# Optimization experiments

Hardware: AMD Instinct MI355X
Metric: run time of the kernel (lower is better)

The kernel has to match this reference:

```python
import jax, jax.numpy as jnp
import numpy as np

# FTDEA(e_hidden=300, r_hidden=100, t_hidden=100)
N_NODES = 50000
N_EDGES = 250000
N_EDGES_ALL = 500000
N_REL = 300
EH, RH, TH = 300, 100, 100


def _seg_softmax(logits, seg, num):
    # torch_geometric.utils.softmax: segment-wise stable softmax
    m = jax.ops.segment_max(logits, seg, num_segments=num)
    e = jnp.exp(logits - m[seg])
    s = jax.ops.segment_sum(e, seg, num_segments=num)
    return e / s[seg]


def _gcn(x, j, i, n):
    deg = jax.ops.segment_sum(jnp.ones(i.shape[0], x.dtype), i, num_segments=n)
    dinv = jnp.where(deg > 0, 1.0 / jnp.sqrt(jnp.maximum(deg, 1.0)), 0.0)
    norm = dinv[j] * dinv[i]
    return jax.nn.relu(jax.ops.segment_sum(norm[:, None] * x[j], i, num_segments=n))


def setup_inputs():
    key = jax.random.key(0)
    ks = jax.random.split(key, 32)
    f32 = jnp.float32

    def w(k, shape):
        return jax.random.normal(k, shape, f32) / np.float32(np.sqrt(shape[0]))

    inp = {
        "x": jax.random.normal(ks[0], (N_NODES, EH), f32),
        "edge_index": jax.random.randint(ks[1], (2, N_EDGES), 0, N_NODES),
        "rel": jax.random.randint(ks[2], (N_EDGES,), 0, N_REL),
        "edge_index_all": jax.random.randint(ks[3], (2, N_EDGES_ALL), 0, N_NODES),
        "rel_size": jnp.arange(N_EDGES),
        "hw1_w": w(ks[4], (EH, EH)), "hw1_b": jnp.zeros((EH,), f32),
        "hw2_w": w(ks[5], (EH, EH)), "hw2_b": jnp.zeros((EH,), f32),
        "tc1_w": w(ks[6], (EH, TH)), "tc1_b": jnp.zeros((TH,), f32),
        "sr1_w": w(ks[7], (2 * TH, RH)), "sr1_b": jnp.zeros((RH,), f32),
        "a1_w": w(ks[8], (RH,)), "a5_w": w(ks[9], (RH,)),
        "wr_w": w(ks[10], (RH + 2 * TH, EH)), "wr_b": jnp.zeros((EH,), f32),
        "wr1_w": w(ks[11], (RH + 2 * TH, EH)), "wr1_b": jnp.zeros((EH,), f32),
        "wr2_w": w(ks[12], (RH + 2 * TH, EH)), "wr2_b": jnp.zeros((EH,), f32),
        "ah_w": w(ks[13], (EH,)), "ah1_w": w(ks[14], (EH,)), "at_w": w(ks[15], (EH,)),
        "ar1_w": w(ks[16], (EH,)), "ar2_w": w(ks[17], (EH,)), "ar3_w": w(ks[18], (EH,)),
        "ai_w": w(ks[19], (EH,)), "aj_w": w(ks[20], (EH,)),
        "fc_w": w(ks[21], (2 * EH,)), "fc_b": jnp.zeros((1,), f32),
    }
    return inp


def _forward(x, hw1_w, hw1_b, hw2_w, hw2_b, tc1_w, tc1_b, sr1_w, sr1_b, a1_w, a5_w,
             wr_w, wr_b, wr1_w, wr1_b, wr2_w, wr2_b, ah_w, ah1_w, at_w,
             ar1_w, ar2_w, ar3_w, ai_w, aj_w, fc_w, fc_b,
             edge_index, rel, edge_index_all, rel_size):
    N = x.shape[0]
    E = rel.shape[0]
    h, t = edge_index[0], edge_index[1]
    j, i = edge_index_all[0], edge_index_all[1]
    lrelu = jax.nn.leaky_relu  # slope 0.01 == F.leaky_relu default

    def highway(x1, x2, wg, bg):
        gate = jax.nn.sigmoid(x1 @ wg + bg)
        return gate * x2 + (1.0 - gate) * x1

    x = highway(x, _gcn(x, j, i, N), hw1_w, hw1_b)
    x = highway(x, _gcn(x, j, i, N), hw2_w, hw2_b)

    # --- GATt_to_R. NB: FTDEA overwrites gat_e_to_r output with zeros, so
    # x_res1 input is all-zeros and GAT_E_to_R is mathematically dead code.
    # Also r_in_t1 aliases r_in_t in the torch code, so the in-place per-relation
    # mean loop rewrites BOTH -> r_in_t1 = per-relation mean features.
    s = x @ tc1_w + tc1_b                                    # [N, t]
    cnt = jnp.maximum(jax.ops.segment_sum(jnp.ones(E, x.dtype), rel, num_segments=N_REL), 1.0)[:, None]
    mh = jax.ops.segment_sum(s[h], rel, num_segments=N_REL) / cnt
    mt = jax.ops.segment_sum(s[t], rel, num_segments=N_REL) / cnt
    r_in_t1 = jnp.concatenate([mh, mt], axis=1)[rel]         # [E, 2t]
    x_res2 = r_in_t1 @ sr1_w + sr1_b                         # [E, r]
    x_res1 = jnp.zeros((E, RH), x.dtype)                     # zeroed GAT_E_to_R output
    e1 = x_res2 @ a1_w + x_res1 @ a5_w                       # [E]
    alpha = _seg_softmax(lrelu(e1), rel, N_REL)
    x_type = jax.ops.segment_sum(alpha[:, None] * x_res2[rel_size], rel, num_segments=N_REL)  # spmm
    r_f = jnp.concatenate([x_res1 + x_type[rel], r_in_t1], axis=1)   # [E, r+2t]

    # --- GATr_to_e: three attention rounds (head, tail, head) ---
    def r2e(x_e, wr, br, a_node, a_rel, idx):
        e_r = r_f @ wr + br                                  # [E, e]
        logits = x_e[idx] @ a_node + e_r @ a_rel             # [E]
        a = _seg_softmax(lrelu(logits), idx, N)
        agg = jax.nn.relu(jax.ops.segment_sum(a[:, None] * e_r[rel_size], idx, num_segments=N))
        return x_e + agg

    x = r2e(x, wr_w, wr_b, ah_w, ar1_w, h)
    x = r2e(x, wr1_w, wr1_b, at_w, ar2_w, t)
    x = r2e(x, wr2_w, wr2_b, ah1_w, ar3_w, h)

    # --- GAT_act over edge_index_all ---
    logits = (x @ ai_w)[i] + (x @ aj_w)[j]
    a = _seg_softmax(lrelu(logits), i, N)
    g = jax.nn.relu(jax.ops.segment_sum(a[:, None] * x[j], i, num_segments=N))

    return jnp.concatenate([x, g], axis=1) @ fc_w + fc_b[0]  # [N]


def reference(x, edge_index, rel, edge_index_all, rel_size, hw1_w, hw1_b, hw2_w, hw2_b,
              tc1_w, tc1_b, sr1_w, sr1_b, a1_w, a5_w, wr_w, wr_b, wr1_w, wr1_b,
              wr2_w, wr2_b, ah_w, ah1_w, at_w, ar1_w, ar2_w, ar3_w, ai_w, aj_w, fc_w, fc_b):
    return _forward(x, hw1_w, hw1_b, hw2_w, hw2_b, tc1_w, tc1_b, sr1_w, sr1_b, a1_w, a5_w,
                    wr_w, wr_b, wr1_w, wr1_b, wr2_w, wr2_b, ah_w, ah1_w, at_w,
                    ar1_w, ar2_w, ar3_w, ai_w, aj_w, fc_w, fc_b,
                    edge_index, rel, edge_index_all, rel_size)
```

## Files before the change

kernel.cpp:

```cpp
#include <hip/hip_runtime.h>
#include <hip/hip_bf16.h>

typedef __hip_bfloat16 bf16;
typedef __attribute__((ext_vector_type(8))) short bf16x8_t;
typedef __attribute__((ext_vector_type(8))) unsigned short u16x8;
typedef __attribute__((ext_vector_type(4))) float f32x4_t;

__device__ __forceinline__ float b2f(bf16 v){ return __bfloat162float(v); }
__device__ __forceinline__ bf16 f2b(float v){ return __float2bfloat16(v); }
__device__ __forceinline__ short tobits(float v){ bf16 b = f2b(v); return *(short*)&b; }
__device__ __forceinline__ float us2f(ushort u){ return __uint_as_float(((unsigned)u)<<16); }
__device__ __forceinline__ ushort f2us(float v){ bf16 b = f2b(v); return *(ushort*)&b; }

#define NN 50000
#define NE 250000
#define NEA 500000
#define NR 300
#define EHD 300
#define THD 100
#define RHD 100
#define XP 320
#define ERP 320
#define RCH 8
#define NBN 98
#define NBR 75

__device__ __forceinline__ int clampi(int v, int n){ return ((unsigned)v < (unsigned)n) ? v : 0; }

__device__ __forceinline__ int rdl_i(int v, int l){ return __builtin_amdgcn_readlane(v, l); }
__device__ __forceinline__ float rdl_f(float v, int l){ return __int_as_float(__builtin_amdgcn_readlane(__float_as_int(v), l)); }

__device__ __forceinline__ float dpp_sum(float x){
    int v;
    v = __builtin_amdgcn_update_dpp(0, __float_as_int(x), 0x111, 0xf, 0xf, true); x += __int_as_float(v);
    v = __builtin_amdgcn_update_dpp(0, __float_as_int(x), 0x112, 0xf, 0xf, true); x += __int_as_float(v);
    v = __builtin_amdgcn_update_dpp(0, __float_as_int(x), 0x114, 0xf, 0xf, true); x += __int_as_float(v);
    v = __builtin_amdgcn_update_dpp(0, __float_as_int(x), 0x118, 0xf, 0xf, true); x += __int_as_float(v);
    v = __builtin_amdgcn_update_dpp(0, __float_as_int(x), 0x142, 0xf, 0xf, true); x += __int_as_float(v);
    v = __builtin_amdgcn_update_dpp(0, __float_as_int(x), 0x143, 0xf, 0xf, true); x += __int_as_float(v);
    return __int_as_float(__builtin_amdgcn_readlane(__float_as_int(x), 63));
}
__device__ __forceinline__ float dpp_max(float x){
    int v;
    v = __builtin_amdgcn_update_dpp(__float_as_int(x), __float_as_int(x), 0x111, 0xf, 0xf, false); x = fmaxf(x, __int_as_float(v));
    v = __builtin_amdgcn_update_dpp(__float_as_int(x), __float_as_int(x), 0x112, 0xf, 0xf, false); x = fmaxf(x, __int_as_float(v));
    v = __builtin_amdgcn_update_dpp(__float_as_int(x), __float_as_int(x), 0x114, 0xf, 0xf, false); x = fmaxf(x, __int_as_float(v));
    v = __builtin_amdgcn_update_dpp(__float_as_int(x), __float_as_int(x), 0x118, 0xf, 0xf, false); x = fmaxf(x, __int_as_float(v));
    v = __builtin_amdgcn_update_dpp(__float_as_int(x), __float_as_int(x), 0x142, 0xf, 0xf, false); x = fmaxf(x, __int_as_float(v));
    v = __builtin_amdgcn_update_dpp(__float_as_int(x), __float_as_int(x), 0x143, 0xf, 0xf, false); x = fmaxf(x, __int_as_float(v));
    return __int_as_float(__builtin_amdgcn_readlane(__float_as_int(x), 63));
}

__global__ void k_prep(const float* __restrict__ xin, ushort* __restrict__ xFu,
                       const float* __restrict__ hw1w, const float* __restrict__ hw2w,
                       const float* __restrict__ tc1w,
                       short* __restrict__ Wt1, short* __restrict__ Wt2, short* __restrict__ Wtc,
                       const float* __restrict__ ahw, const float* __restrict__ atw,
                       const float* __restrict__ ah1w, const float* __restrict__ ajw,
                       const float* __restrict__ aiw, const float* __restrict__ fcw,
                       float* __restrict__ apad, int* __restrict__ bcnt){
    int i = blockIdx.x*256 + threadIdx.x;
    if(i < 512) bcnt[i] = 0;
    const int NC = NN*40;
    const int S1 = NC + 320*320;
    const int S2 = S1 + 320*320;
    const int S3 = S2 + 128*320;
    const int S4 = S3 + 7*XP;
    if(i < NC){
        int nrow = i/40, c8 = i - nrow*40, c = c8*8;
        ushort o[8];
        if(c + 8 <= EHD){
            const float4* src = (const float4*)(xin + (size_t)nrow*EHD + c);
            float4 v0 = src[0], v1 = src[1];
            o[0]=f2us(v0.x); o[1]=f2us(v0.y); o[2]=f2us(v0.z); o[3]=f2us(v0.w);
            o[4]=f2us(v1.x); o[5]=f2us(v1.y); o[6]=f2us(v1.z); o[7]=f2us(v1.w);
        } else {
            #pragma unroll
            for(int k=0;k<8;k++){
                int cc = c + k;
                o[k] = (cc < EHD) ? f2us(xin[(size_t)nrow*EHD + cc]) : (ushort)0;
            }
        }
        u16x8 w;
        #pragma unroll
        for(int k=0;k<8;k++) w[k] = o[k];
        *(u16x8*)(xFu + (size_t)nrow*XP + c) = w;
    } else if(i < S1){
        int ii = i - NC; int n = ii/320, k = ii - n*320;
        Wt1[ii] = (n < EHD && k < EHD) ? tobits(hw1w[(size_t)k*EHD + n]) : (short)0;
    } else if(i < S2){
        int ii = i - S1; int n = ii/320, k = ii - n*320;
        Wt2[ii] = (n < EHD && k < EHD) ? tobits(hw2w[(size_t)k*EHD + n]) : (short)0;
    } else if(i < S3){
        int ii = i - S2; int n = ii/320, k = ii - n*320;
        Wtc[ii] = (n < THD && k < EHD) ? tobits(tc1w[(size_t)k*THD + n]) : (short)0;
    } else if(i < S4){
        int ii = i - S3; int v = ii/XP, c = ii - v*XP;
        float val = 0.f;
        if(c < EHD){
            const float* src = (v==0)?ahw:(v==1)?atw:(v==2)?ah1w:(v==3)?ajw:(v==4)?aiw:
                               (v==5)? fcw : (fcw + EHD);
            val = src[c];
        }
        apad[ii] = val;
    }
}

__global__ __launch_bounds__(256) void k_bincnt(const int* __restrict__ ji, const int* __restrict__ ht,
                         const int* __restrict__ rel, int* __restrict__ bcnt){
    int s = blockIdx.y;
    int n_s = (s == 0) ? NEA : NE;
    int base_e = blockIdx.x*2048;
    if(base_e >= n_s) return;
    int shift = (s < 3) ? 9 : 2;
    int tid = threadIdx.x;
    __shared__ int h[128];
    if(tid < 128) h[tid] = 0;
    __syncthreads();
    #pragma unroll
    for(int u=0;u<8;u++){
        int e = base_e + u*256 + tid;
        if(e < n_s){
            int key;
            if(s == 0) key = clampi(ji[NEA + e], NN);
            else if(s == 1) key = clampi(ht[e], NN);
            else if(s == 2) key = clampi(ht[NE + e], NN);
            else key = clampi(rel[e], NR);
            atomicAdd(&h[key >> shift], 1);
        }
    }
    __syncthreads();
    if(tid < 128 && h[tid] > 0) atomicAdd(&bcnt[s*128 + tid], h[tid]);
}

__global__ void k_bscan(const int* __restrict__ bcnt, int* __restrict__ gbase, int* __restrict__ gcur){
    __shared__ int lds[512];
    int tid = threadIdx.x;
    int v = bcnt[tid];
    lds[tid] = v; __syncthreads();
    for(int st=1; st<128; st<<=1){
        int add = ((tid & 127) >= st) ? lds[tid-st] : 0;
        __syncthreads();
        lds[tid] += add;
        __syncthreads();
    }
    int s = tid >> 7, b = tid & 127;
    int excl = lds[tid] - v;
    gbase[s*129 + b] = excl;
    gcur[s*128 + b] = excl;
    if(b == 127) gbase[s*129 + 128] = lds[tid];
}

__global__ __launch_bounds__(256) void k_bin(const int* __restrict__ ji, const int* __restrict__ ht,
                      const int* __restrict__ rel, int* __restrict__ gcur,
                      int2* __restrict__ t0, int2* __restrict__ t1,
                      int2* __restrict__ t2, int2* __restrict__ t3){
    int s = blockIdx.y;
    int n_s = (s == 0) ? NEA : NE;
    int base_e = blockIdx.x*2048;
    if(base_e >= n_s) return;
    int shift = (s < 3) ? 9 : 2;
    int tid = threadIdx.x;
    __shared__ int cnt[128], lof[128], base[128];
    __shared__ int2 buf[2048];
    if(tid < 128) cnt[tid] = 0;
    __syncthreads();
    int kk[8], pp[8], bb[8], ss[8];
    #pragma unroll
    for(int u=0;u<8;u++){
        int e = base_e + u*256 + tid;
        bb[u] = -1;
        if(e < n_s){
            int key, pay;
            if(s == 0){ key = clampi(ji[NEA + e], NN); pay = clampi(ji[e], NN); }
            else if(s == 1){ key = clampi(ht[e], NN); pay = clampi(rel[e], NR); }
            else if(s == 2){ key = clampi(ht[NE + e], NN); pay = clampi(rel[e], NR); }
            else { key = clampi(rel[e], NR); pay = e; }
            int b = key >> shift;
            kk[u] = key; pp[u] = pay; bb[u] = b;
            ss[u] = atomicAdd(&cnt[b], 1);
        }
    }
    __syncthreads();
    if(tid == 0){
        int run = 0;
        for(int b=0;b<128;b++){ lof[b] = run; run += cnt[b]; }
    }
    __syncthreads();
    #pragma unroll
    for(int u=0;u<8;u++){
        if(bb[u] >= 0){
            int pos = lof[bb[u]] + ss[u];
            buf[pos] = make_int2(kk[u], pp[u]);
        }
    }
    __syncthreads();
    if(tid < 128 && cnt[tid] > 0) base[tid] = atomicAdd(&gcur[s*128 + tid], cnt[tid]);
    __syncthreads();
    int2* tmp = (s==0) ? t0 : (s==1) ? t1 : (s==2) ? t2 : t3;
    int total = lof[127] + cnt[127];
    for(int idx=tid; idx<total; idx+=256){
        int2 kp = buf[idx];
        int b = kp.x >> shift;
        tmp[base[b] + (idx - lof[b])] = kp;
    }
}

__global__ __launch_bounds__(256) void k_place(const int* __restrict__ gbase,
                        const int2* __restrict__ t0, const int2* __restrict__ t1,
                        const int2* __restrict__ t2, const int2* __restrict__ t3,
                        int* __restrict__ off_all, int* __restrict__ off_h,
                        int* __restrict__ off_t, int* __restrict__ off_r,
                        int* __restrict__ adj_all, int* __restrict__ adj_h,
                        int* __restrict__ adj_t, int* __restrict__ adj_r,
                        float* __restrict__ dinv){
    int s = blockIdx.y, b = blockIdx.x;
    int NB = (s < 3) ? NBN : NBR;
    if(b >= NB) return;
    int W = (s < 3) ? 512 : 4;
    int len = (s < 3) ? NN : NR;
    const int2* tmp = (s==0) ? t0 : (s==1) ? t1 : (s==2) ? t2 : t3;
    int* off = (s==0) ? off_all : (s==1) ? off_h : (s==2) ? off_t : off_r;
    int* adj = (s==0) ? adj_all : (s==1) ? adj_h : (s==2) ? adj_t : adj_r;
    int node0 = b*W;
    int node1 = node0 + W; if(node1 > len) node1 = len;
    int nloc = node1 - node0;
    int wstart = gbase[s*129 + b], wend = gbase[s*129 + b + 1];
    __shared__ int hist[512];
    __shared__ int cur[512];
    __shared__ int sb[256];
    int tid = threadIdx.x;
    for(int k=tid; k<nloc; k+=256) hist[k] = 0;
    __syncthreads();
    for(int idx = wstart + tid; idx < wend; idx += 256){
        int local = tmp[idx].x - node0;
        if((unsigned)local < (unsigned)nloc) atomicAdd(&hist[local], 1);
    }
    __syncthreads();
    int v0 = (2*tid   < nloc) ? hist[2*tid]   : 0;
    int v1 = (2*tid+1 < nloc) ? hist[2*tid+1] : 0;
    int ps = v0 + v1;
    sb[tid] = ps; __syncthreads();
    for(int st=1; st<256; st<<=1){
        int add = (tid >= st) ? sb[tid-st] : 0;
        __syncthreads();
        sb[tid] += add;
        __syncthreads();
    }
    int excl = sb[tid] - ps;
    if(2*tid < nloc){
        int o = wstart + excl;
        off[node0 + 2*tid] = o;
        cur[2*tid] = o;
        if(s == 0) dinv[node0 + 2*tid] = v0 > 0 ? rsqrtf((float)v0) : 0.f;
    }
    if(2*tid+1 < nloc){
        int o = wstart + excl + v0;
        off[node0 + 2*tid+1] = o;
        cur[2*tid+1] = o;
        if(s == 0) dinv[node0 + 2*tid+1] = v1 > 0 ? rsqrtf((float)v1) : 0.f;
    }
    if(b == NB-1 && tid == 0) off[len] = gbase[s*129 + 128];
    __syncthreads();
    for(int idx = wstart + tid; idx < wend; idx += 256){
        int2 kp = tmp[idx];
        int local = kp.x - node0;
        if((unsigned)local < (unsigned)nloc){
            int slot = atomicAdd(&cur[local], 1);
            adj[slot] = kp.y;
        }
    }
}

__global__ void k_gcn(const bf16* __restrict__ xs, bf16* __restrict__ xd,
                      const int* __restrict__ off, const int* __restrict__ adjj,
                      const float* __restrict__ dinv){
    int wid = threadIdx.x >> 6, lane = threadIdx.x & 63;
    int n = blockIdx.x*4 + wid;
    if(n >= NN) return;
    float di = dinv[n];
    int s0 = off[n], s1 = off[n+1], cnt = s1 - s0;
    bool act = lane < 40;
    float c0=0,c1=0,c2=0,c3=0,c4=0,c5=0,c6=0,c7=0;
    if(cnt > 0 && cnt <= 64){
        int jl = (lane < cnt) ? clampi(adjj[s0+lane], NN) : 0;
        float dl = (lane < cnt) ? dinv[jl] : 0.f;
        int it = 0;
        for(; it+4 <= cnt; it += 4){
            int j0=rdl_i(jl,it), j1=rdl_i(jl,it+1), j2=rdl_i(jl,it+2), j3=rdl_i(jl,it+3);
            float n0=di*rdl_f(dl,it), n1=di*rdl_f(dl,it+1), n2=di*rdl_f(dl,it+2), n3=di*rdl_f(dl,it+3);
            if(act){
                u16x8 v0 = ((const u16x8*)(xs + (size_t)j0*XP))[lane];
                u16x8 v1 = ((const u16x8*)(xs + (size_t)j1*XP))[lane];
                u16x8 v2 = ((const u16x8*)(xs + (size_t)j2*XP))[lane];
                u16x8 v3 = ((const u16x8*)(xs + (size_t)j3*XP))[lane];
                c0 += n0*us2f(v0[0])+n1*us2f(v1[0])+n2*us2f(v2[0])+n3*us2f(v3[0]);
                c1 += n0*us2f(v0[1])+n1*us2f(v1[1])+n2*us2f(v2[1])+n3*us2f(v3[1]);
                c2 += n0*us2f(v0[2])+n1*us2f(v1[2])+n2*us2f(v2[2])+n3*us2f(v3[2]);
                c3 += n0*us2f(v0[3])+n1*us2f(v1[3])+n2*us2f(v2[3])+n3*us2f(v3[3]);
                c4 += n0*us2f(v0[4])+n1*us2f(v1[4])+n2*us2f(v2[4])+n3*us2f(v3[4]);
                c5 += n0*us2f(v0[5])+n1*us2f(v1[5])+n2*us2f(v2[5])+n3*us2f(v3[5]);
                c6 += n0*us2f(v0[6])+n1*us2f(v1[6])+n2*us2f(v2[6])+n3*us2f(v3[6]);
                c7 += n0*us2f(v0[7])+n1*us2f(v1[7])+n2*us2f(v2[7])+n3*us2f(v3[7]);
            }
        }
        for(; it < cnt; it++){
            int j0 = rdl_i(jl, it);
            float n0 = di*rdl_f(dl, it);
            if(act){
                u16x8 v0 = ((const u16x8*)(xs + (size_t)j0*XP))[lane];
                c0 += n0*us2f(v0[0]); c1 += n0*us2f(v0[1]); c2 += n0*us2f(v0[2]); c3 += n0*us2f(v0[3]);
                c4 += n0*us2f(v0[4]); c5 += n0*us2f(v0[5]); c6 += n0*us2f(v0[6]); c7 += n0*us2f(v0[7]);
            }
        }
    } else if(cnt > 64){
        for(int it=s0; it<s1; it++){
            int j = clampi(adjj[it], NN);
            float nr = di * dinv[j];
            if(act){
                u16x8 v0 = ((const u16x8*)(xs + (size_t)j*XP))[lane];
                c0 += nr*us2f(v0[0]); c1 += nr*us2f(v0[1]); c2 += nr*us2f(v0[2]); c3 += nr*us2f(v0[3]);
                c4 += nr*us2f(v0[4]); c5 += nr*us2f(v0[5]); c6 += nr*us2f(v0[6]); c7 += nr*us2f(v0[7]);
            }
        }
    }
    if(act){
        u16x8 w;
        w[0]=f2us(fmaxf(c0,0.f)); w[1]=f2us(fmaxf(c1,0.f)); w[2]=f2us(fmaxf(c2,0.f)); w[3]=f2us(fmaxf(c3,0.f));
        w[4]=f2us(fmaxf(c4,0.f)); w[5]=f2us(fmaxf(c5,0.f)); w[6]=f2us(fmaxf(c6,0.f)); w[7]=f2us(fmaxf(c7,0.f));
        ((u16x8*)(xd + (size_t)n*XP))[lane] = w;
    }
}

template<int MODE>
__global__ __launch_bounds__(256) void k_gemm_mfma(const bf16* __restrict__ X,
                       const short* __restrict__ Wt, const float* __restrict__ bias,
                       bf16* __restrict__ out, const bf16* __restrict__ Xprev,
                       int M, int K, int Ncols, int ldOut){
    __shared__ short As[64][40];
    __shared__ short Bs[64][40];
    int tid = threadIdx.x;
    int bm = blockIdx.x*64, bn = blockIdx.y*64;
    int wid = tid>>6, lane = tid&63;
    int wm = (wid&1)*32, wn = (wid>>1)*32;
    int lm = lane&15, lq = lane>>4;
    f32x4_t acc00={0,0,0,0}, acc01={0,0,0,0}, acc10={0,0,0,0}, acc11={0,0,0,0};
    int mrow = tid>>2, kc = (tid&3)*8;
    bool fullM = (bm + 64 <= M);
    union U8 { bf16x8_t v; uint2 u[2]; };
    for(int k0=0; k0<K; k0+=32){
        {
            int gm = bm + mrow;
            U8 a;
            if(fullM || gm < M){
                const uint2* src = (const uint2*)(X + (size_t)gm*K + k0 + kc);
                a.u[0] = src[0]; a.u[1] = src[1];
            } else { a.u[0] = {0,0}; a.u[1] = {0,0}; }
            *(bf16x8_t*)&As[mrow][kc] = a.v;
        }
        {
            U8 b;
            const uint2* src = (const uint2*)(Wt + (size_t)(bn + mrow)*K + k0 + kc);
            b.u[0] = src[0]; b.u[1] = src[1];
            *(bf16x8_t*)&Bs[mrow][kc] = b.v;
        }
        __syncthreads();
        bf16x8_t a0 = *(bf16x8_t*)&As[wm + lm][lq*8];
        bf16x8_t a1 = *(bf16x8_t*)&As[wm + 16 + lm][lq*8];
        bf16x8_t b0 = *(bf16x8_t*)&Bs[wn + lm][lq*8];
        bf16x8_t b1 = *(bf16x8_t*)&Bs[wn + 16 + lm][lq*8];
        acc00 = __builtin_amdgcn_mfma_f32_16x16x32_bf16(a0, b0, acc00, 0, 0, 0);
        acc01 = __builtin_amdgcn_mfma_f32_16x16x32_bf16(a0, b1, acc01, 0, 0, 0);
        acc10 = __builtin_amdgcn_mfma_f32_16x16x32_bf16(a1, b0, acc10, 0, 0, 0);
        acc11 = __builtin_amdgcn_mfma_f32_16x16x32_bf16(a1, b1, acc11, 0, 0, 0);
        __syncthreads();
    }
    #pragma unroll
    for(int tm=0;tm<2;tm++){
        #pragma unroll
        for(int tn=0;tn<2;tn++){
            f32x4_t a = tm==0 ? (tn==0 ? acc00 : acc01) : (tn==0 ? acc10 : acc11);
            int gn = bn + wn + tn*16 + lm;
            if(gn >= Ncols) continue;
            float bi = bias[gn];
            #pragma unroll
            for(int r=0;r<4;r++){
                int gm = bm + wm + tm*16 + lq*4 + r;
                if(gm >= M) continue;
                float t = a[r] + bi;
                size_t p = (size_t)gm*ldOut + gn;
                if(MODE == 0){
                    out[p] = f2b(t);
                } else {
                    float g = __builtin_amdgcn_rcpf(1.f + __expf(-t));
                    out[p] = f2b(g*b2f(out[p]) + (1.f - g)*b2f(Xprev[p]));
                }
            }
        }
    }
}

__global__ void k_relsum2(const bf16* __restrict__ s, const int* __restrict__ ht,
                          const int* __restrict__ off_r, const int* __restrict__ adj_r,
                          float* __restrict__ RFpart){
    int r = blockIdx.x, c = blockIdx.y, d = threadIdx.x;
    if(d >= THD) return;
    int s0 = off_r[r], s1 = off_r[r+1];
    int cnt = s1 - s0;
    float ah = 0.f, at2 = 0.f;
    if(cnt > 0){
        int per = (cnt + RCH - 1)/RCH;
        int lo = s0 + c*per, hi = lo + per; if(hi > s1) hi = s1;
        for(int it=lo; it<hi; it++){
            int e = clampi(adj_r[it], NE);
            int hh = clampi(ht[e], NN), tt = clampi(ht[NE + e], NN);
            ah  += b2f(s[(size_t)hh*THD + d]);
            at2 += b2f(s[(size_t)tt*THD + d]);
        }
    }
    size_t base = (size_t)(r*RCH + c)*2*THD;
    RFpart[base + d] = ah;
    RFpart[base + THD + d] = at2;
}

__global__ void k_relfin(const float* __restrict__ sr1w, const float* __restrict__ sr1b,
                         const int* __restrict__ off_r, const float* __restrict__ RFpart,
                         float* __restrict__ RF){
    int r = blockIdx.x, d = threadIdx.x;
    int cnt = off_r[r+1] - off_r[r];
    float inv = 1.f/(float)(cnt > 1 ? cnt : 1);
    if(d < THD){
        float a = 0.f, b = 0.f;
        #pragma unroll
        for(int c=0;c<RCH;c++){
            size_t base = (size_t)(r*RCH + c)*2*THD;
            a += RFpart[base + d];
            b += RFpart[base + THD + d];
        }
        RF[(size_t)r*EHD + THD   + d] = a*inv;
        RF[(size_t)r*EHD + 2*THD + d] = b*inv;
    }
    __syncthreads();
    if(d < RHD){
        float v = 0.f;
        if(cnt > 0){
            v = sr1b[d];
            for(int k2=0; k2<2*THD; k2++) v += RF[(size_t)r*EHD + THD + k2] * sr1w[k2*RHD + d];
        }
        RF[(size_t)r*EHD + d] = v;
    }
}

__global__ void k_reler(const float* __restrict__ RF,
                        const float* w0, const float* b0, const float* w1, const float* b1,
                        const float* w2, const float* b2,
                        const float* ar1, const float* ar2, const float* ar3,
                        float* __restrict__ ER, float* __restrict__ cvec){
    int r = blockIdx.x, kk = blockIdx.y;
    const float* w = kk==0 ? w0 : (kk==1 ? w1 : w2);
    const float* b = kk==0 ? b0 : (kk==1 ? b1 : b2);
    const float* a = kk==0 ? ar1 : (kk==1 ? ar2 : ar3);
    int tid = threadIdx.x;
    __shared__ float rfs[EHD];
    for(int d=tid; d<EHD; d+=256) rfs[d] = RF[(size_t)r*EHD + d];
    __syncthreads();
    float pd = 0.f;
    for(int o = tid; o < ERP; o += 256){
        float v = 0.f;
        if(o < EHD){
            v = b[o];
            for(int d=0; d<EHD; d++) v += rfs[d] * w[(size_t)d*EHD + o];
            pd += v * a[o];
        }
        ER[((size_t)kk*NR + r)*ERP + o] = v;
    }
    __shared__ float red[4];
    pd = dpp_sum(pd);
    if((tid & 63) == 0) red[tid>>6] = pd;
    __syncthreads();
    if(tid == 0) cvec[kk*NR + r] = red[0]+red[1]+red[2]+red[3];
}

__device__ __forceinline__ void r2e_round(float* xv, bool act, int lane, int s0, int s1,
        int rl, float cval,
        const int* __restrict__ adjrel, const float* __restrict__ ERk,
        const float* __restrict__ ck, const float* __restrict__ an){
    float p = 0.f;
    if(act){
        const float4* a4 = (const float4*)an;
        float4 a0 = a4[2*lane], a1 = a4[2*lane+1];
        p = xv[0]*a0.x + xv[1]*a0.y + xv[2]*a0.z + xv[3]*a0.w
          + xv[4]*a1.x + xv[5]*a1.y + xv[6]*a1.z + xv[7]*a1.w;
    }
    p = dpp_sum(p);
    int cnt = s1 - s0;
    if(cnt <= 0) return;
    float c0=0,c1=0,c2=0,c3=0,c4=0,c5=0,c6=0,c7=0;
    if(cnt <= 64){
        float lg = p + cval;
        lg = lg > 0 ? lg : 0.01f*lg;
        float mx = dpp_max((lane < cnt) ? lg : -1e30f);
        float ex = (lane < cnt) ? __expf(lg - mx) : 0.f;
        float al = ex * __builtin_amdgcn_rcpf(dpp_sum(ex));
        int it = 0;
        for(; it+2 <= cnt; it += 2){
            int r0i = rdl_i(rl, it), r1i = rdl_i(rl, it+1);
            float q0 = rdl_f(al, it), q1 = rdl_f(al, it+1);
            if(act){
                const float4* e0p = (const float4*)(ERk + (size_t)r0i*ERP);
                const float4* e1p = (const float4*)(ERk + (size_t)r1i*ERP);
                float4 e0 = e0p[2*lane], e1 = e1p[2*lane];
                float4 f0 = e0p[2*lane+1], f1 = e1p[2*lane+1];
                c0 += q0*e0.x + q1*e1.x; c1 += q0*e0.y + q1*e1.y;
                c2 += q0*e0.z + q1*e1.z; c3 += q0*e0.w + q1*e1.w;
                c4 += q0*f0.x + q1*f1.x; c5 += q0*f0.y + q1*f1.y;
                c6 += q0*f0.z + q1*f1.z; c7 += q0*f0.w + q1*f1.w;
            }
        }
        if(it < cnt){
            int r0i = rdl_i(rl, it);
            float q0 = rdl_f(al, it);
            if(act){
                const float4* e0p = (const float4*)(ERk + (size_t)r0i*ERP);
                float4 e0 = e0p[2*lane], f0 = e0p[2*lane+1];
                c0 += q0*e0.x; c1 += q0*e0.y; c2 += q0*e0.z; c3 += q0*e0.w;
                c4 += q0*f0.x; c5 += q0*f0.y; c6 += q0*f0.z; c7 += q0*f0.w;
            }
        }
    } else {
        float mx = -1e30f;
        for(int it=s0; it<s1; it++){
            float lg = p + ck[clampi(adjrel[it], NR)];
            lg = lg > 0 ? lg : 0.01f*lg;
            mx = fmaxf(mx, lg);
        }
        float ssum = 0.f;
        for(int it=s0; it<s1; it++){
            float lg = p + ck[clampi(adjrel[it], NR)];
            lg = lg > 0 ? lg : 0.01f*lg;
            ssum += __expf(lg - mx);
        }
        float rinv = __builtin_amdgcn_rcpf(ssum);
        for(int it=s0; it<s1; it++){
            int r = clampi(adjrel[it], NR);
            float lg = p + ck[r];
            lg = lg > 0 ? lg : 0.01f*lg;
            float aw = __expf(lg - mx)*rinv;
            if(act){
                const float4* er4 = (const float4*)(ERk + (size_t)r*ERP);
                float4 e0 = er4[2*lane], f0 = er4[2*lane+1];
                c0 += aw*e0.x; c1 += aw*e0.y; c2 += aw*e0.z; c3 += aw*e0.w;
                c4 += aw*f0.x; c5 += aw*f0.y; c6 += aw*f0.z; c7 += aw*f0.w;
            }
        }
    }
    xv[0] += fmaxf(c0,0.f); xv[1] += fmaxf(c1,0.f); xv[2] += fmaxf(c2,0.f); xv[3] += fmaxf(c3,0.f);
    xv[4] += fmaxf(c4,0.f); xv[5] += fmaxf(c5,0.f); xv[6] += fmaxf(c6,0.f); xv[7] += fmaxf(c7,0.f);
}

__global__ void k_r2e3(bf16* __restrict__ x,
                       const int* __restrict__ off_h, const int* __restrict__ adj_h,
                       const int* __restrict__ off_t, const int* __restrict__ adj_t,
                       const float* __restrict__ ER, const float* __restrict__ cvec,
                       const float* __restrict__ apad, float* __restrict__ ajv){
    int wid = threadIdx.x >> 6, lane = threadIdx.x & 63;
    int n = blockIdx.x*4 + wid;
    if(n >= NN) return;
    bool act = lane < 40;
    u16x8* xr = (u16x8*)(x + (size_t)n*XP);
    float xv[8];
    if(act){
        u16x8 v = xr[lane];
        #pragma unroll
        for(int k=0;k<8;k++) xv[k] = us2f(v[k]);
    } else {
        #pragma unroll
        for(int k=0;k<8;k++) xv[k] = 0.f;
    }
    int h0 = off_h[n], h1 = off_h[n+1];
    int t0_ = off_t[n], t1_ = off_t[n+1];
    int hcnt = h1 - h0, tcnt = t1_ - t0_;
    int rlh = (hcnt > 0 && hcnt <= 64 && lane < hcnt) ? clampi(adj_h[h0+lane], NR) : 0;
    int rlt = (tcnt > 0 && tcnt <= 64 && lane < tcnt) ? clampi(adj_t[t0_+lane], NR) : 0;
    float ch1 = cvec[rlh], ctv = cvec[NR + rlt], ch3 = cvec[2*NR + rlh];
    r2e_round(xv, act, lane, h0, h1, rlh, ch1, adj_h, ER,                    cvec,      apad);
    r2e_round(xv, act, lane, t0_, t1_, rlt, ctv, adj_t, ER + (size_t)NR*ERP, cvec+NR,   apad + XP);
    r2e_round(xv, act, lane, h0, h1, rlh, ch3, adj_h, ER + (size_t)2*NR*ERP, cvec+2*NR, apad + 2*XP);
    {
        float p = 0.f;
        if(act){
            const float4* a4 = (const float4*)(apad + 3*XP);
            float4 a0 = a4[2*lane], a1 = a4[2*lane+1];
            p = xv[0]*a0.x + xv[1]*a0.y + xv[2]*a0.z + xv[3]*a0.w
              + xv[4]*a1.x + xv[5]*a1.y + xv[6]*a1.z + xv[7]*a1.w;
        }
        p = dpp_sum(p);
        if(lane == 0) ajv[n] = p;
    }
    if(act){
        u16x8 w;
        #pragma unroll
        for(int k=0;k<8;k++) w[k] = f2us(xv[k]);
        xr[lane] = w;
    }
}

__global__ void k_final(const bf16* __restrict__ x, const float* __restrict__ ajv,
                        const int* __restrict__ off, const int* __restrict__ adjj,
                        const float* __restrict__ apad, const float* __restrict__ fcb,
                        float* __restrict__ out){
    int wid = threadIdx.x >> 6, lane = threadIdx.x & 63;
    int n = blockIdx.x*4 + wid;
    if(n >= NN) return;
    bool act = lane < 40;
    float xv[8];
    if(act){
        u16x8 v = ((const u16x8*)(x + (size_t)n*XP))[lane];
        #pragma unroll
        for(int k=0;k<8;k++) xv[k] = us2f(v[k]);
    } else {
        #pragma unroll
        for(int k=0;k<8;k++) xv[k] = 0.f;
    }
    float p = 0.f;
    if(act){
        const float4* a4 = (const float4*)(apad + 4*XP);
        float4 a0 = a4[2*lane], a1 = a4[2*lane+1];
        p = xv[0]*a0.x + xv[1]*a0.y + xv[2]*a0.z + xv[3]*a0.w
          + xv[4]*a1.x + xv[5]*a1.y + xv[6]*a1.z + xv[7]*a1.w;
    }
    p = dpp_sum(p);
    int s0 = off[n], s1 = off[n+1], cnt = s1 - s0;
    float c0=0,c1=0,c2=0,c3=0,c4=0,c5=0,c6=0,c7=0;
    if(cnt > 0 && cnt <= 64){
        int jl = (lane < cnt) ? clampi(adjj[s0+lane], NN) : 0;
        float av = (lane < cnt) ? ajv[jl] : 0.f;
        float lg = p + av;
        lg = lg > 0 ? lg : 0.01f*lg;
        float mx = dpp_max((lane < cnt) ? lg : -1e30f);
        float ex = (lane < cnt) ? __expf(lg - mx) : 0.f;
        float al = ex * __builtin_amdgcn_rcpf(dpp_sum(ex));
        int it = 0;
        for(; it+4 <= cnt; it += 4){
            int j0=rdl_i(jl,it), j1=rdl_i(jl,it+1), j2=rdl_i(jl,it+2), j3=rdl_i(jl,it+3);
            float q0=rdl_f(al,it), q1=rdl_f(al,it+1), q2=rdl_f(al,it+2), q3=rdl_f(al,it+3);
            if(act){
                u16x8 v0 = ((const u16x8*)(x + (size_t)j0*XP))[lane];
                u16x8 v1 = ((const u16x8*)(x + (size_t)j1*XP))[lane];
                u16x8 v2 = ((const u16x8*)(x + (size_t)j2*XP))[lane];
                u16x8 v3 = ((const u16x8*)(x + (size_t)j3*XP))[lane];
                c0 += q0*us2f(v0[0])+q1*us2f(v1[0])+q2*us2f(v2[0])+q3*us2f(v3[0]);
                c1 += q0*us2f(v0[1])+q1*us2f(v1[1])+q2*us2f(v2[1])+q3*us2f(v3[1]);
                c2 += q0*us2f(v0[2])+q1*us2f(v1[2])+q2*us2f(v2[2])+q3*us2f(v3[2]);
                c3 += q0*us2f(v0[3])+q1*us2f(v1[3])+q2*us2f(v2[3])+q3*us2f(v3[3]);
                c4 += q0*us2f(v0[4])+q1*us2f(v1[4])+q2*us2f(v2[4])+q3*us2f(v3[4]);
                c5 += q0*us2f(v0[5])+q1*us2f(v1[5])+q2*us2f(v2[5])+q3*us2f(v3[5]);
                c6 += q0*us2f(v0[6])+q1*us2f(v1[6])+q2*us2f(v2[6])+q3*us2f(v3[6]);
                c7 += q0*us2f(v0[7])+q1*us2f(v1[7])+q2*us2f(v2[7])+q3*us2f(v3[7]);
            }
        }
        for(; it < cnt; it++){
            int j0 = rdl_i(jl, it);
            float q0 = rdl_f(al, it);
            if(act){
                u16x8 v0 = ((const u16x8*)(x + (size_t)j0*XP))[lane];
                c0 += q0*us2f(v0[0]); c1 += q0*us2f(v0[1]); c2 += q0*us2f(v0[2]); c3 += q0*us2f(v0[3]);
                c4 += q0*us2f(v0[4]); c5 += q0*us2f(v0[5]); c6 += q0*us2f(v0[6]); c7 += q0*us2f(v0[7]);
            }
        }
    } else if(cnt > 64){
        float mx = -1e30f;
        for(int it=s0; it<s1; it++){
            float lg = p + ajv[clampi(adjj[it], NN)];
            lg = lg > 0 ? lg : 0.01f*lg;
            mx = fmaxf(mx, lg);
        }
        float ssum = 0.f;
        for(int it=s0; it<s1; it++){
            float lg = p + ajv[clampi(adjj[it], NN)];
            lg = lg > 0 ? lg : 0.01f*lg;
            ssum += __expf(lg - mx);
        }
        float rinv = __builtin_amdgcn_rcpf(ssum);
        for(int it=s0; it<s1; it++){
            int j = clampi(adjj[it], NN);
            float lg = p + ajv[j];
            lg = lg > 0 ? lg : 0.01f*lg;
            float aw = __expf(lg - mx)*rinv;
            if(act){
                u16x8 v0 = ((const u16x8*)(x + (size_t)j*XP))[lane];
                c0 += aw*us2f(v0[0]); c1 += aw*us2f(v0[1]); c2 += aw*us2f(v0[2]); c3 += aw*us2f(v0[3]);
                c4 += aw*us2f(v0[4]); c5 += aw*us2f(v0[5]); c6 += aw*us2f(v0[6]); c7 += aw*us2f(v0[7]);
            }
        }
    }
    float part = 0.f;
    if(act){
        const float4* f5 = (const float4*)(apad + 5*XP);
        const float4* f6 = (const float4*)(apad + 6*XP);
        float4 u0 = f5[2*lane], u1 = f5[2*lane+1];
        float4 g0 = f6[2*lane], g1 = f6[2*lane+1];
        part = xv[0]*u0.x + xv[1]*u0.y + xv[2]*u0.z + xv[3]*u0.w
             + xv[4]*u1.x + xv[5]*u1.y + xv[6]*u1.z + xv[7]*u1.w
             + fmaxf(c0,0.f)*g0.x + fmaxf(c1,0.f)*g0.y + fmaxf(c2,0.f)*g0.z + fmaxf(c3,0.f)*g0.w
             + fmaxf(c4,0.f)*g1.x + fmaxf(c5,0.f)*g1.y + fmaxf(c6,0.f)*g1.z + fmaxf(c7,0.f)*g1.w;
    }
    part = dpp_sum(part);
    if(lane == 0) out[n] = part + fcb[0];
}

extern "C" void kernel_launch(void* const* d_in, const int* in_sizes, int n_in,
                              void* d_out, int out_size, void* d_ws, size_t ws_size,
                              hipStream_t stream){
    const float* x_in = (const float*)d_in[0];
    const int*  ht   = (const int*)d_in[1];
    const int*  rel  = (const int*)d_in[2];
    const int*  ji   = (const int*)d_in[3];
    const float* hw1w=(const float*)d_in[5];  const float* hw1b=(const float*)d_in[6];
    const float* hw2w=(const float*)d_in[7];  const float* hw2b=(const float*)d_in[8];
    const float* tc1w=(const float*)d_in[9];  const float* tc1b=(const float*)d_in[10];
    const float* sr1w=(const float*)d_in[11]; const float* sr1b=(const float*)d_in[12];
    const float* wrw =(const float*)d_in[15]; const float* wrb =(const float*)d_in[16];
    const float* wr1w=(const float*)d_in[17]; const float* wr1b=(const float*)d_in[18];
    const float* wr2w=(const float*)d_in[19]; const float* wr2b=(const float*)d_in[20];
    const float* ahw =(const float*)d_in[21]; const float* ah1w=(const float*)d_in[22];
    const float* atw =(const float*)d_in[23];
    const float* ar1 =(const float*)d_in[24]; const float* ar2 =(const float*)d_in[25];
    const float* ar3 =(const float*)d_in[26];
    const float* aiw =(const float*)d_in[27]; const float* ajw =(const float*)d_in[28];
    const float* fcw =(const float*)d_in[29]; const float* fcb =(const float*)d_in[30];
    float* out = (float*)d_out;

    char* w = (char*)d_ws;
    auto alloc = [&](size_t bytes)->char*{ char* p = w; w += (bytes + 255)/256*256; return p; };
    bf16* xF = (bf16*)alloc((size_t)NN*XP*2);
    bf16* B  = (bf16*)alloc((size_t)NN*XP*2);
    char* Bc = (char*)B;
    int2* tmp_all = (int2*)(Bc);
    int2* tmp_h   = (int2*)(Bc + 4u*1024*1024);
    int2* tmp_t   = (int2*)(Bc + 8u*1024*1024);
    int2* tmp_r   = (int2*)(Bc + 12u*1024*1024);
    bf16*  sbuf   = (bf16*)(Bc);
    float* RF     = (float*)(Bc + 10u*1024*1024);
    float* RFpart = (float*)(Bc + 11u*1024*1024);
    float* ER     = (float*)(Bc + 13u*1024*1024);
    float* cvec   = (float*)(Bc + 14u*1024*1024 + 512u*1024);
    float* ajv    = (float*)(Bc + 15u*1024*1024);
    short* Wt1 = (short*)alloc((size_t)320*320*2);
    short* Wt2 = (short*)alloc((size_t)320*320*2);
    short* Wtc = (short*)alloc((size_t)128*320*2);
    float* apad = (float*)alloc((size_t)7*XP*4);
    float* dinv = (float*)alloc((size_t)NN*4);
    int* off_all=(int*)alloc((NN+1)*4);
    int* adj_all=(int*)alloc((size_t)NEA*4);
    int* off_h  =(int*)alloc((NN+1)*4);
    int* adj_h  =(int*)alloc((size_t)NE*4);
    int* off_t  =(int*)alloc((NN+1)*4);
    int* adj_t  =(int*)alloc((size_t)NE*4);
    int* off_r  =(int*)alloc((NR+1)*4);
    int* adj_r  =(int*)alloc((size_t)NE*4);
    int* bcnt   =(int*)alloc(512*4);
    int* gbase  =(int*)alloc(4*129*4);
    int* gcur   =(int*)alloc(4*128*4);

    const int PRT = NN*40 + 2*320*320 + 128*320 + 7*XP;
    k_prep<<<dim3((PRT+255)/256), dim3(256), 0, stream>>>(x_in, (ushort*)xF, hw1w, hw2w, tc1w,
                                                          Wt1, Wt2, Wtc,
                                                          ahw, atw, ah1w, ajw, aiw, fcw,
                                                          apad, bcnt);
    k_bincnt<<<dim3((NEA+2047)/2048, 4), dim3(256), 0, stream>>>(ji, ht, rel, bcnt);
    k_bscan<<<dim3(1), dim3(512), 0, stream>>>(bcnt, gbase, gcur);
    k_bin<<<dim3((NEA+2047)/2048, 4), dim3(256), 0, stream>>>(ji, ht, rel, gcur,
                                                              tmp_all, tmp_h, tmp_t, tmp_r);
    k_place<<<dim3(NBN, 4), dim3(256), 0, stream>>>(gbase, tmp_all, tmp_h, tmp_t, tmp_r,
                                                    off_all, off_h, off_t, off_r,
                                                    adj_all, adj_h, adj_t, adj_r, dinv);

    const int nb4 = (NN+3)/4;
    const dim3 gg((NN+63)/64, (EHD+63)/64);
    k_gcn<<<dim3(nb4), dim3(256), 0, stream>>>(xF, B, off_all, adj_all, dinv);
    k_gemm_mfma<1><<<gg, dim3(256), 0, stream>>>(xF, Wt1, hw1b, B, xF, NN, XP, EHD, XP);
    k_gcn<<<dim3(nb4), dim3(256), 0, stream>>>(B, xF, off_all, adj_all, dinv);
    k_gemm_mfma<1><<<gg, dim3(256), 0, stream>>>(B, Wt2, hw2b, xF, B, NN, XP, EHD, XP);
    k_gemm_mfma<0><<<dim3((NN+63)/64, (THD+63)/64), dim3(256), 0, stream>>>(xF, Wtc, tc1b, sbuf, xF, NN, XP, THD, THD);
    k_relsum2<<<dim3(NR, RCH), dim3(128), 0, stream>>>(sbuf, ht, off_r, adj_r, RFpart);
    k_relfin<<<dim3(NR), dim3(128), 0, stream>>>(sr1w, sr1b, off_r, RFpart, RF);
    k_reler<<<dim3(NR, 3), dim3(256), 0, stream>>>(RF, wrw, wrb, wr1w, wr1b, wr2w, wr2b,
                                                   ar1, ar2, ar3, ER, cvec);
    k_r2e3<<<dim3(nb4), dim3(256), 0, stream>>>(xF, off_h, adj_h, off_t, adj_t, ER, cvec,
                                                apad, ajv);
    k_final<<<dim3(nb4), dim3(256), 0, stream>>>(xF, ajv, off_all, adj_all, apad, fcb, out);
}
```

Measured before the change: 630.4 us.

## Enlarge MFMA GEMM tiles to 128x128 with direct global-to-LDS loads and unroll gathers

Moves the bf16 MFMA GEMM from 64x64 tiles to 128x128 tiles, with a 4x4 accumulator grid per wave, XOR-swizzled LDS and global_load_lds async copies. Buffers and padded weights are enlarged so the boundary checks can be dropped. The GCN and final GAT gather loops also gain an 8-wide unrolled path so more row loads are in flight. The trade-off is higher register pressure and padding work, and the larger tiles give fewer blocks for the 100-column GEMM.

```diff
diff --git a/kernel.cpp b/kernel.cpp
--- a/kernel.cpp
+++ b/kernel.cpp
@@ -13,6 +13,7 @@
 __device__ __forceinline__ ushort f2us(float v){ bf16 b = f2b(v); return *(ushort*)&b; }
 
 #define NN 50000
+#define NN128 50048
 #define NE 250000
 #define NEA 500000
 #define NR 300
@@ -30,6 +31,12 @@
 __device__ __forceinline__ int rdl_i(int v, int l){ return __builtin_amdgcn_readlane(v, l); }
 __device__ __forceinline__ float rdl_f(float v, int l){ return __int_as_float(__builtin_amdgcn_readlane(__float_as_int(v), l)); }
 
+typedef const __attribute__((address_space(1))) unsigned int* gas1_t;
+typedef __attribute__((address_space(3))) unsigned int* las3_t;
+__device__ __forceinline__ void glds16(const void* g, void* l){
+    __builtin_amdgcn_global_load_lds((gas1_t)g, (las3_t)l, 16, 0, 0);
+}
+
 __device__ __forceinline__ float dpp_sum(float x){
     int v;
     v = __builtin_amdgcn_update_dpp(0, __float_as_int(x), 0x111, 0xf, 0xf, true); x += __int_as_float(v);
@@ -62,8 +69,8 @@
     int i = blockIdx.x*256 + threadIdx.x;
     if(i < 512) bcnt[i] = 0;
     const int NC = NN*40;
-    const int S1 = NC + 320*320;
-    const int S2 = S1 + 320*320;
+    const int S1 = NC + 384*320;
+    const int S2 = S1 + 384*320;
     const int S3 = S2 + 128*320;
     const int S4 = S3 + 7*XP;
     if(i < NC){
@@ -286,6 +293,30 @@
         int jl = (lane < cnt) ? clampi(adjj[s0+lane], NN) : 0;
         float dl = (lane < cnt) ? dinv[jl] : 0.f;
         int it = 0;
+        for(; it+8 <= cnt; it += 8){
+            int j0=rdl_i(jl,it),   j1=rdl_i(jl,it+1), j2=rdl_i(jl,it+2), j3=rdl_i(jl,it+3);
+            int j4=rdl_i(jl,it+4), j5=rdl_i(jl,it+5), j6=rdl_i(jl,it+6), j7=rdl_i(jl,it+7);
+            float n0=di*rdl_f(dl,it),   n1=di*rdl_f(dl,it+1), n2=di*rdl_f(dl,it+2), n3=di*rdl_f(dl,it+3);
+            float n4=di*rdl_f(dl,it+4), n5=di*rdl_f(dl,it+5), n6=di*rdl_f(dl,it+6), n7=di*rdl_f(dl,it+7);
+            if(act){
+                u16x8 v0 = ((const u16x8*)(xs + (size_t)j0*XP))[lane];
+                u16x8 v1 = ((const u16x8*)(xs + (size_t)j1*XP))[lane];
+                u16x8 v2 = ((const u16x8*)(xs + (size_t)j2*XP))[lane];
+                u16x8 v3 = ((const u16x8*)(xs + (size_t)j3*XP))[lane];
+                u16x8 v4 = ((const u16x8*)(xs + (size_t)j4*XP))[lane];
+                u16x8 v5 = ((const u16x8*)(xs + (size_t)j5*XP))[lane];
+                u16x8 v6 = ((const u16x8*)(xs + (size_t)j6*XP))[lane];
+                u16x8 v7 = ((const u16x8*)(xs + (size_t)j7*XP))[lane];
+                c0 += n0*us2f(v0[0])+n1*us2f(v1[0])+n2*us2f(v2[0])+n3*us2f(v3[0])+n4*us2f(v4[0])+n5*us2f(v5[0])+n6*us2f(v6[0])+n7*us2f(v7[0]);
+                c1 += n0*us2f(v0[1])+n1*us2f(v1[1])+n2*us2f(v2[1])+n3*us2f(v3[1])+n4*us2f(v4[1])+n5*us2f(v5[1])+n6*us2f(v6[1])+n7*us2f(v7[1]);
+                c2 += n0*us2f(v0[2])+n1*us2f(v1[2])+n2*us2f(v2[2])+n3*us2f(v3[2])+n4*us2f(v4[2])+n5*us2f(v5[2])+n6*us2f(v6[2])+n7*us2f(v7[2]);
+                c3 += n0*us2f(v0[3])+n1*us2f(v1[3])+n2*us2f(v2[3])+n3*us2f(v3[3])+n4*us2f(v4[3])+n5*us2f(v5[3])+n6*us2f(v6[3])+n7*us2f(v7[3]);
+                c4 += n0*us2f(v0[4])+n1*us2f(v1[4])+n2*us2f(v2[4])+n3*us2f(v3[4])+n4*us2f(v4[4])+n5*us2f(v5[4])+n6*us2f(v6[4])+n7*us2f(v7[4]);
+                c5 += n0*us2f(v0[5])+n1*us2f(v1[5])+n2*us2f(v2[5])+n3*us2f(v3[5])+n4*us2f(v4[5])+n5*us2f(v5[5])+n6*us2f(v6[5])+n7*us2f(v7[5]);
+                c6 += n0*us2f(v0[6])+n1*us2f(v1[6])+n2*us2f(v2[6])+n3*us2f(v3[6])+n4*us2f(v4[6])+n5*us2f(v5[6])+n6*us2f(v6[6])+n7*us2f(v7[6]);
+                c7 += n0*us2f(v0[7])+n1*us2f(v1[7])+n2*us2f(v2[7])+n3*us2f(v3[7])+n4*us2f(v4[7])+n5*us2f(v5[7])+n6*us2f(v6[7])+n7*us2f(v7[7]);
+            }
+        }
         for(; it+4 <= cnt; it += 4){
             int j0=rdl_i(jl,it), j1=rdl_i(jl,it+1), j2=rdl_i(jl,it+2), j3=rdl_i(jl,it+3);
             float n0=di*rdl_f(dl,it), n1=di*rdl_f(dl,it+1), n2=di*rdl_f(dl,it+2), n3=di*rdl_f(dl,it+3);
@@ -337,57 +368,66 @@
                        const short* __restrict__ Wt, const float* __restrict__ bias,
                        bf16* __restrict__ out, const bf16* __restrict__ Xprev,
                        int M, int K, int Ncols, int ldOut){
-    __shared__ short As[64][40];
-    __shared__ short Bs[64][40];
+    __shared__ short As[128*32];
+    __shared__ short Bs[128*32];
     int tid = threadIdx.x;
-    int bm = blockIdx.x*64, bn = blockIdx.y*64;
+    int bm = blockIdx.x*128, bn = blockIdx.y*128;
     int wid = tid>>6, lane = tid&63;
-    int wm = (wid&1)*32, wn = (wid>>1)*32;
+    int wm = (wid&1)*64, wn = (wid>>1)*64;
     int lm = lane&15, lq = lane>>4;
-    f32x4_t acc00={0,0,0,0}, acc01={0,0,0,0}, acc10={0,0,0,0}, acc11={0,0,0,0};
-    int mrow = tid>>2, kc = (tid&3)*8;
-    bool fullM = (bm + 64 <= M);
-    union U8 { bf16x8_t v; uint2 u[2]; };
+    f32x4_t acc[4][4];
+    #pragma unroll
+    for(int i=0;i<4;i++)
+        #pragma unroll
+        for(int j=0;j<4;j++) acc[i][j] = f32x4_t{0.f,0.f,0.f,0.f};
+    int r0 = tid>>2, sl = tid&3;
+    int r1 = 64 + r0;
+    int sl0 = sl ^ ((r0>>1)&3);
+    int sl1 = sl ^ ((r1>>1)&3);
+    short* baseA0 = As + (size_t)(wid*64)*8;
+    short* baseA1 = As + (size_t)(256 + wid*64)*8;
+    short* baseB0 = Bs + (size_t)(wid*64)*8;
+    short* baseB1 = Bs + (size_t)(256 + wid*64)*8;
+    const bf16* gA0 = X  + (size_t)(bm + r0)*K + sl0*8;
+    const bf16* gA1 = X  + (size_t)(bm + r1)*K + sl1*8;
+    const short* gB0 = Wt + (size_t)(bn + r0)*K + sl0*8;
+    const short* gB1 = Wt + (size_t)(bn + r1)*K + sl1*8;
     for(int k0=0; k0<K; k0+=32){
-        {
-            int gm = bm + mrow;
-            U8 a;
-            if(fullM || gm < M){
-                const uint2* src = (const uint2*)(X + (size_t)gm*K + k0 + kc);
-                a.u[0] = src[0]; a.u[1] = src[1];
-            } else { a.u[0] = {0,0}; a.u[1] = {0,0}; }
-            *(bf16x8_t*)&As[mrow][kc] = a.v;
-        }
-        {
-            U8 b;
-            const uint2* src = (const uint2*)(Wt + (size_t)(bn + mrow)*K + k0 + kc);
-            b.u[0] = src[0]; b.u[1] = src[1];
-            *(bf16x8_t*)&Bs[mrow][kc] = b.v;
-        }
+        glds16(gA0 + k0, baseA0);
+        glds16(gA1 + k0, baseA1);
+        glds16(gB0 + k0, baseB0);
+        glds16(gB1 + k0, baseB1);
         __syncthreads();
-        bf16x8_t a0 = *(bf16x8_t*)&As[wm + lm][lq*8];
-        bf16x8_t a1 = *(bf16x8_t*)&As[wm + 16 + lm][lq*8];
-        bf16x8_t b0 = *(bf16x8_t*)&Bs[wn + lm][lq*8];
-        bf16x8_t b1 = *(bf16x8_t*)&Bs[wn + 16 + lm][lq*8];
-        acc00 = __builtin_amdgcn_mfma_f32_16x16x32_bf16(a0, b0, acc00, 0, 0, 0);
-        acc01 = __builtin_amdgcn_mfma_f32_16x16x32_bf16(a0, b1, acc01, 0, 0, 0);
-        acc10 = __builtin_amdgcn_mfma_f32_16x16x32_bf16(a1, b0, acc10, 0, 0, 0);
-        acc11 = __builtin_amdgcn_mfma_f32_16x16x32_bf16(a1, b1, acc11, 0, 0, 0);
+        bf16x8_t a[4], b[4];
+        #pragma unroll
+        for(int mi=0;mi<4;mi++){
+            int r = wm + mi*16 + lm;
+            a[mi] = *(const bf16x8_t*)(As + r*32 + ((lq ^ ((r>>1)&3))*8));
+        }
+        #pragma unroll
+        for(int ni=0;ni<4;ni++){
+            int r = wn + ni*16 + lm;
+            b[ni] = *(const bf16x8_t*)(Bs + r*32 + ((lq ^ ((r>>1)&3))*8));
+        }
+        #pragma unroll
+        for(int mi=0;mi<4;mi++)
+            #pragma unroll
+            for(int ni=0;ni<4;ni++)
+                acc[mi][ni] = __builtin_amdgcn_mfma_f32_16x16x32_bf16(a[mi], b[ni], acc[mi][ni], 0, 0, 0);
         __syncthreads();
     }
     #pragma unroll
-    for(int tm=0;tm<2;tm++){
-        #pragma unroll
-        for(int tn=0;tn<2;tn++){
-            f32x4_t a = tm==0 ? (tn==0 ? acc00 : acc01) : (tn==0 ? acc10 : acc11);
-            int gn = bn + wn + tn*16 + lm;
+    for(int mi=0;mi<4;mi++){
+        #pragma unroll
+        for(int ni=0;ni<4;ni++){
+            int gn = bn + wn + ni*16 + lm;
             if(gn >= Ncols) continue;
             float bi = bias[gn];
             #pragma unroll
             for(int r=0;r<4;r++){
-                int gm = bm + wm + tm*16 + lq*4 + r;
+                int gm = bm + wm + mi*16 + lq*4 + r;
                 if(gm >= M) continue;
-                float t = a[r] + bi;
+                float t = acc[mi][ni][r] + bi;
                 size_t p = (size_t)gm*ldOut + gn;
                 if(MODE == 0){
                     out[p] = f2b(t);
@@ -641,6 +681,30 @@
         float ex = (lane < cnt) ? __expf(lg - mx) : 0.f;
         float al = ex * __builtin_amdgcn_rcpf(dpp_sum(ex));
         int it = 0;
+        for(; it+8 <= cnt; it += 8){
+            int j0=rdl_i(jl,it),   j1=rdl_i(jl,it+1), j2=rdl_i(jl,it+2), j3=rdl_i(jl,it+3);
+            int j4=rdl_i(jl,it+4), j5=rdl_i(jl,it+5), j6=rdl_i(jl,it+6), j7=rdl_i(jl,it+7);
+            float q0=rdl_f(al,it),   q1=rdl_f(al,it+1), q2=rdl_f(al,it+2), q3=rdl_f(al,it+3);
+            float q4=rdl_f(al,it+4), q5=rdl_f(al,it+5), q6=rdl_f(al,it+6), q7=rdl_f(al,it+7);
+            if(act){
+                u16x8 v0 = ((const u16x8*)(x + (size_t)j0*XP))[lane];
+                u16x8 v1 = ((const u16x8*)(x + (size_t)j1*XP))[lane];
+                u16x8 v2 = ((const u16x8*)(x + (size_t)j2*XP))[lane];
+                u16x8 v3 = ((const u16x8*)(x + (size_t)j3*XP))[lane];
+                u16x8 v4 = ((const u16x8*)(x + (size_t)j4*XP))[lane];
+                u16x8 v5 = ((const u16x8*)(x + (size_t)j5*XP))[lane];
+                u16x8 v6 = ((const u16x8*)(x + (size_t)j6*XP))[lane];
+                u16x8 v7 = ((const u16x8*)(x + (size_t)j7*XP))[lane];
+                c0 += q0*us2f(v0[0])+q1*us2f(v1[0])+q2*us2f(v2[0])+q3*us2f(v3[0])+q4*us2f(v4[0])+q5*us2f(v5[0])+q6*us2f(v6[0])+q7*us2f(v7[0]);
+                c1 += q0*us2f(v0[1])+q1*us2f(v1[1])+q2*us2f(v2[1])+q3*us2f(v3[1])+q4*us2f(v4[1])+q5*us2f(v5[1])+q6*us2f(v6[1])+q7*us2f(v7[1]);
+                c2 += q0*us2f(v0[2])+q1*us2f(v1[2])+q2*us2f(v2[2])+q3*us2f(v3[2])+q4*us2f(v4[2])+q5*us2f(v5[2])+q6*us2f(v6[2])+q7*us2f(v7[2]);
+                c3 += q0*us2f(v0[3])+q1*us2f(v1[3])+q2*us2f(v2[3])+q3*us2f(v3[3])+q4*us2f(v4[3])+q5*us2f(v5[3])+q6*us2f(v6[3])+q7*us2f(v7[3]);
+                c4 += q0*us2f(v0[4])+q1*us2f(v1[4])+q2*us2f(v2[4])+q3*us2f(v3[4])+q4*us2f(v4[4])+q5*us2f(v5[4])+q6*us2f(v6[4])+q7*us2f(v7[4]);
+                c5 += q0*us2f(v0[5])+q1*us2f(v1[5])+q2*us2f(v2[5])+q3*us2f(v3[5])+q4*us2f(v4[5])+q5*us2f(v5[5])+q6*us2f(v6[5])+q7*us2f(v7[5]);
+                c6 += q0*us2f(v0[6])+q1*us2f(v1[6])+q2*us2f(v2[6])+q3*us2f(v3[6])+q4*us2f(v4[6])+q5*us2f(v5[6])+q6*us2f(v6[6])+q7*us2f(v7[6]);
+                c7 += q0*us2f(v0[7])+q1*us2f(v1[7])+q2*us2f(v2[7])+q3*us2f(v3[7])+q4*us2f(v4[7])+q5*us2f(v5[7])+q6*us2f(v6[7])+q7*us2f(v7[7]);
+            }
+        }
         for(; it+4 <= cnt; it += 4){
             int j0=rdl_i(jl,it), j1=rdl_i(jl,it+1), j2=rdl_i(jl,it+2), j3=rdl_i(jl,it+3);
             float q0=rdl_f(al,it), q1=rdl_f(al,it+1), q2=rdl_f(al,it+2), q3=rdl_f(al,it+3);
@@ -733,21 +797,21 @@
 
     char* w = (char*)d_ws;
     auto alloc = [&](size_t bytes)->char*{ char* p = w; w += (bytes + 255)/256*256; return p; };
-    bf16* xF = (bf16*)alloc((size_t)NN*XP*2);
-    bf16* B  = (bf16*)alloc((size_t)NN*XP*2);
+    bf16* xF = (bf16*)alloc((size_t)NN128*XP*2);
+    bf16* B  = (bf16*)alloc((size_t)NN128*XP*2);
     char* Bc = (char*)B;
     int2* tmp_all = (int2*)(Bc);
     int2* tmp_h   = (int2*)(Bc + 4u*1024*1024);
     int2* tmp_t   = (int2*)(Bc + 8u*1024*1024);
     int2* tmp_r   = (int2*)(Bc + 12u*1024*1024);
     bf16*  sbuf   = (bf16*)(Bc);
-    float* RF     = (float*)(Bc + 10u*1024*1024);
-    float* RFpart = (float*)(Bc + 11u*1024*1024);
-    float* ER     = (float*)(Bc + 13u*1024*1024);
-    float* cvec   = (float*)(Bc + 14u*1024*1024 + 512u*1024);
-    float* ajv    = (float*)(Bc + 15u*1024*1024);
-    short* Wt1 = (short*)alloc((size_t)320*320*2);
-    short* Wt2 = (short*)alloc((size_t)320*320*2);
+    float* RF     = (float*)(Bc + 11u*1024*1024);
+    float* RFpart = (float*)(Bc + 12u*1024*1024);
+    float* ER     = (float*)(Bc + 14u*1024*1024);
+    float* cvec   = (float*)(Bc + 15u*1024*1024 + 512u*1024);
+    float* ajv    = (float*)(Bc + 16u*1024*1024);
+    short* Wt1 = (short*)alloc((size_t)384*320*2);
+    short* Wt2 = (short*)alloc((size_t)384*320*2);
     short* Wtc = (short*)alloc((size_t)128*320*2);
     float* apad = (float*)alloc((size_t)7*XP*4);
     float* dinv = (float*)alloc((size_t)NN*4);
@@ -763,7 +827,7 @@
     int* gbase  =(int*)alloc(4*129*4);
     int* gcur   =(int*)alloc(4*128*4);
 
-    const int PRT = NN*40 + 2*320*320 + 128*320 + 7*XP;
+    const int PRT = NN*40 + 2*384*320 + 128*320 + 7*XP;
     k_prep<<<dim3((PRT+255)/256), dim3(256), 0, stream>>>(x_in, (ushort*)xF, hw1w, hw2w, tc1w,
                                                           Wt1, Wt2, Wtc,
                                                           ahw, atw, ah1w, ajw, aiw, fcw,
@@ -777,12 +841,12 @@
                                                     adj_all, adj_h, adj_t, adj_r, dinv);
 
     const int nb4 = (NN+3)/4;
-    const dim3 gg((NN+63)/64, (EHD+63)/64);
+    const dim3 gg((NN+127)/128, (EHD+127)/128);
     k_gcn<<<dim3(nb4), dim3(256), 0, stream>>>(xF, B, off_all, adj_all, dinv);
     k_gemm_mfma<1><<<gg, dim3(256), 0, stream>>>(xF, Wt1, hw1b, B, xF, NN, XP, EHD, XP);
     k_gcn<<<dim3(nb4), dim3(256), 0, stream>>>(B, xF, off_all, adj_all, dinv);
     k_gemm_mfma<1><<<gg, dim3(256), 0, stream>>>(B, Wt2, hw2b, xF, B, NN, XP, EHD, XP);
-    k_gemm_mfma<0><<<dim3((NN+63)/64, (THD+63)/64), dim3(256), 0, stream>>>(xF, Wtc, tc1b, sbuf, xF, NN, XP, THD, THD);
+    k_gemm_mfma<0><<<dim3((NN+127)/128, 1), dim3(256), 0, stream>>>(xF, Wtc, tc1b, sbuf, xF, NN, XP, THD, THD);
     k_relsum2<<<dim3(NR, RCH), dim3(128), 0, stream>>>(sbuf, ht, off_r, adj_r, RFpart);
     k_relfin<<<dim3(NR), dim3(128), 0, stream>>>(sr1w, sr1b, off_r, RFpart, RF);
     k_reler<<<dim3(NR, 3), dim3(256), 0, stream>>>(RF, wrw, wrb, wr1w, wr1b, wr2w, wr2b,
```

Measured after the change: 671.9 us. 6.6% more time.
